# Optimization experiments

Measured on AMD Instinct MI355X. Metric: run time of the kernel, lower is better.

Reference implementation:

```python
import jax, jax.numpy as jnp
import numpy as np

B, C, H, W = 8, 32, 256, 448


def setup_inputs() -> dict:
    key = jax.random.key(0)
    k1, k2 = jax.random.split(key)
    input1 = jax.random.normal(k1, (B, C, H, W), dtype=jnp.float32)
    input2 = jax.random.normal(k2, (B, 2, H, W), dtype=jnp.float32)  # flow (u, v)
    return {"input1": input1, "input2": input2, "kernel_size": 1}


def _forward_splat(input1, input2):
    """Forward warp: splat each source pixel to (x+u, y+v) with bilinear weights,
    accumulating via scatter-add (kernel_size=1 -> 2x2 bilinear footprint)."""
    b, c, h, w = input1.shape
    u = input2[:, 0]  # [B,H,W] horizontal flow
    v = input2[:, 1]  # [B,H,W] vertical flow
    xs = jnp.arange(w, dtype=input2.dtype)
    ys = jnp.arange(h, dtype=input2.dtype)
    tx = xs[None, None, :] + u  # target x, [B,H,W]
    ty = ys[None, :, None] + v  # target y, [B,H,W]
    x0 = jnp.floor(tx).astype(jnp.int32)
    y0 = jnp.floor(ty).astype(jnp.int32)
    fx = tx - x0.astype(tx.dtype)
    fy = ty - y0.astype(ty.dtype)

    vals = input1.transpose(0, 2, 3, 1).reshape(b * h * w, c)  # [BHW, C]
    out = jnp.zeros((b * h * w, c), dtype=input1.dtype)
    batch_off = (jnp.arange(b, dtype=jnp.int32) * (h * w))[:, None, None]

    for dx, dy in ((0, 0), (1, 0), (0, 1), (1, 1)):
        xx = x0 + dx
        yy = y0 + dy
        wx = fx if dx == 1 else (1.0 - fx)
        wy = fy if dy == 1 else (1.0 - fy)
        wgt = wx * wy  # [B,H,W]
        valid = (xx >= 0) & (xx < w) & (yy >= 0) & (yy < h)
        wgt = jnp.where(valid, wgt, 0.0)
        idx = batch_off + jnp.clip(yy, 0, h - 1) * w + jnp.clip(xx, 0, w - 1)
        out = out.at[idx.reshape(-1)].add(wgt.reshape(-1, 1) * vals)

    return out.reshape(b, h, w, c).transpose(0, 3, 1, 2)


def reference(input1, input2, kernel_size):
    # kernel_size=1 corresponds to the standard bilinear (2x2) splat footprint.
    return _forward_splat(input1, input2)
```

## Files before the change

kernel.cpp:

```cpp
#include <hip/hip_runtime.h>
#include <hip/hip_fp16.h>

constexpr int B = 8;
constexpr int C = 32;
constexpr int H = 256;
constexpr int W = 448;
constexpr int HW = H * W;

constexpr int TW  = 32;
constexpr int TH  = 16;
constexpr int RAD = 3;
constexpr int WX  = TW + 2 * RAD;
constexpr int WY  = TH + 2 * RAD;
constexpr int NSRC = WX * WY;
constexpr int NT  = 512;
constexpr int SITER = (NSRC + NT - 1) / NT;

static __device__ __forceinline__ unsigned pkrtz(float a, float b) {
    return __builtin_bit_cast(unsigned, __builtin_amdgcn_cvt_pkrtz(a, b));
}

static __device__ __forceinline__ __half2 h2(unsigned u) {
    union { unsigned u; __half2 h; } x;
    x.u = u;
    return x.h;
}

__global__ __launch_bounds__(NT)
void splat_out(const float* __restrict__ in1,
               const float* __restrict__ flow,
               float* __restrict__ out,
               unsigned* __restrict__ wcnt,
               unsigned* __restrict__ wlist,
               unsigned cap) {
    __shared__ unsigned geomR[NSRC];
    __shared__ unsigned geomW[2 * NSRC];
    __shared__ uint4    valV[4 * NSRC];

    int bid = blockIdx.x;
    int b = bid & 7;
    int t = bid >> 3;
    int ty = t / 14;
    int tx = t - ty * 14;
    int ox = tx * TW, oy = ty * TH;
    int tid = threadIdx.x;
    int qlx = tid & 31, qly = tid >> 5;
    int qx = ox + qlx, qy = oy + qly;

    int sg[SITER];
    const int fbase = b * 2 * HW;
#pragma unroll
    for (int j = 0; j < SITER; ++j) {
        int i = tid + j * NT;
        if (i < NSRC) {
            int wy = i / WX, wx = i - wy * WX;
            int sx = ox + wx - RAD, sy = oy + wy - RAD;
            int cx = min(max(sx, 0), W - 1), cy = min(max(sy, 0), H - 1);
            int g = cy * W + cx;
            sg[j] = g;
            unsigned gr = 0xFFu, wlo = 0u, whi = 0u;
            if (sx == cx && sy == cy) {
                float u = flow[fbase + g];
                float v = flow[fbase + g + HW];
                float txf = (float)sx + u;
                float tyf = (float)sy + v;
                float x0f = floorf(txf), y0f = floorf(tyf);
                int rx = (int)x0f - sx, ry = (int)y0f - sy;
                if (rx >= -RAD && rx <= RAD - 1 && ry >= -RAD && ry <= RAD - 1) {
                    float fx = txf - x0f, fy = tyf - y0f;
                    wlo = pkrtz((1.f - fx) * (1.f - fy), fx * (1.f - fy));
                    whi = pkrtz((1.f - fx) * fy,         fx * fy);
                    gr = (unsigned)(rx + RAD) | ((unsigned)(ry + RAD) << 3);
                } else if (wx >= RAD && wx < RAD + TW && wy >= RAD && wy < RAD + TH) {
                    unsigned slot = atomicAdd(wcnt, 1u);
                    if (slot < cap) wlist[slot] = ((unsigned)b << 17) | (unsigned)g;
                }
            }
            geomR[i] = gr;
            geomW[2 * i]     = wlo;
            geomW[2 * i + 1] = whi;
        }
    }
    __syncthreads();

    const float* inb = in1 + (size_t)b * C * HW;
#pragma unroll
    for (int j = 0; j < SITER; ++j) {
        int i = tid + j * NT;
        if (i < NSRC) {
            const float* p = inb + sg[j];
#pragma unroll
            for (int q = 0; q < 4; ++q) {
                const float* pq = p + (size_t)(8 * q) * HW;
                uint4 vq;
                vq.x = pkrtz(pq[0],              pq[(size_t)HW]);
                vq.y = pkrtz(pq[(size_t)2 * HW], pq[(size_t)3 * HW]);
                vq.z = pkrtz(pq[(size_t)4 * HW], pq[(size_t)5 * HW]);
                vq.w = pkrtz(pq[(size_t)6 * HW], pq[(size_t)7 * HW]);
                valV[4 * i + q] = vq;
            }
        }
    }

    unsigned long long mAll = 0ull, mDx = 0ull, mDy = 0ull;
    const int qbase = (qly + RAD) * WX + (qlx + RAD);
#pragma unroll
    for (int dy = -RAD; dy <= RAD; ++dy) {
#pragma unroll
        for (int dx = -RAD; dx <= RAD; ++dx) {
            unsigned g = geomR[qbase + dy * WX + dx];
            int tX = (int)(g & 7u) + dx;
            int tY = (int)((g >> 3) & 0x1Fu) + dy;
            bool mx = (unsigned)(tX - 2) <= 1u;
            bool my = (unsigned)(tY - 2) <= 1u;
            const int j = (dy + RAD) * 8 + (dx + RAD);
            unsigned long long bit = (mx && my) ? (1ull << j) : 0ull;
            mAll |= bit;
            if (!(tX & 1)) mDx |= bit;
            if (!(tY & 1)) mDy |= bit;
        }
    }
    __syncthreads();

    __half2 acc2[16];
#pragma unroll
    for (int k = 0; k < 16; ++k) acc2[k] = h2(0u);

    const int joff = 3 * WX + 3;
    unsigned long long m = mAll;
    while (m) {
        int j = (int)__builtin_ctzll(m);
        m &= m - 1;
        int wi = qbase + ((j >> 3) * WX + (j & 7)) - joff;
        unsigned dyy = (unsigned)(mDy >> j) & 1u;
        unsigned dxx = (unsigned)(mDx >> j) & 1u;
        unsigned wd = geomW[2 * wi + dyy];
        unsigned hw = (wd >> (16u * dxx)) & 0xFFFFu;
        __half2 w2 = h2(hw | (hw << 16));
#pragma unroll
        for (int q = 0; q < 4; ++q) {
            uint4 v = valV[4 * wi + q];
            acc2[4 * q + 0] = __hfma2(h2(v.x), w2, acc2[4 * q + 0]);
            acc2[4 * q + 1] = __hfma2(h2(v.y), w2, acc2[4 * q + 1]);
            acc2[4 * q + 2] = __hfma2(h2(v.z), w2, acc2[4 * q + 2]);
            acc2[4 * q + 3] = __hfma2(h2(v.w), w2, acc2[4 * q + 3]);
        }
    }

    float* o = out + (size_t)b * C * HW + qy * W + qx;
#pragma unroll
    for (int k = 0; k < 16; ++k) {
        int c0 = 8 * (k >> 2) + 2 * (k & 3);
        float2 f = __half22float2(acc2[k]);
        o[(size_t)c0 * HW]       = f.x;
        o[(size_t)(c0 + 1) * HW] = f.y;
    }
}

__global__ void outlier_list(const float* __restrict__ in1,
                             const float* __restrict__ flow,
                             float* __restrict__ out,
                             const unsigned* __restrict__ wcnt,
                             const unsigned* __restrict__ wlist,
                             unsigned cap) {
    unsigned n = *wcnt;
    if (n > cap) return;
    unsigned total = n * 8u;
    for (unsigned idx = blockIdx.x * blockDim.x + threadIdx.x;
         idx < total; idx += gridDim.x * blockDim.x) {
        unsigned e = wlist[idx >> 3];
        int c0 = (int)(idx & 7u) * 4;
        int bb = (int)(e >> 17);
        int p  = (int)(e & 0x1FFFFu);
        int y = p / W, x = p - y * W;

        float u = flow[(bb * 2 + 0) * HW + p];
        float v = flow[(bb * 2 + 1) * HW + p];
        float txf = (float)x + u;
        float tyf = (float)y + v;
        float fx0 = floorf(txf), fy0 = floorf(tyf);
        int x0 = (int)fx0, y0 = (int)fy0;
        float fx = txf - fx0, fy = tyf - fy0;
        float w00 = (1.0f - fx) * (1.0f - fy);
        float w10 = fx * (1.0f - fy);
        float w01 = (1.0f - fx) * fy;
        float w11 = fx * fy;
        bool vx0 = (x0 >= 0) && (x0 < W);
        bool vx1 = (x0 + 1 >= 0) && (x0 + 1 < W);
        bool vy0 = (y0 >= 0) && (y0 < H);
        bool vy1 = (y0 + 1 >= 0) && (y0 + 1 < H);
        long o00 = (long)y0 * W + x0;

        const float* src  = in1 + (size_t)bb * C * HW + (size_t)c0 * HW + p;
        float*       dstb = out + (size_t)bb * C * HW + (size_t)c0 * HW;
        for (int c = 0; c < 4; ++c) {
            float val = src[(size_t)c * HW];
            float* ob = dstb + (size_t)c * HW;
            if (vx0 && vy0) atomicAdd(ob + o00,         w00 * val);
            if (vx1 && vy0) atomicAdd(ob + o00 + 1,     w10 * val);
            if (vx0 && vy1) atomicAdd(ob + o00 + W,     w01 * val);
            if (vx1 && vy1) atomicAdd(ob + o00 + W + 1, w11 * val);
        }
    }
}

__global__ void outlier_fallback(const float* __restrict__ in1,
                                 const float* __restrict__ flow,
                                 float* __restrict__ out,
                                 const unsigned* __restrict__ wcnt,
                                 unsigned cap) {
    if (*wcnt <= cap) return;
    int npix = B * HW;
    for (int idx = blockIdx.x * blockDim.x + threadIdx.x;
         idx < npix; idx += gridDim.x * blockDim.x) {
        int b = idx / HW;
        int p = idx - b * HW;
        int y = p / W, x = p - y * W;
        float u = flow[(b * 2 + 0) * HW + p];
        float v = flow[(b * 2 + 1) * HW + p];
        float txf = (float)x + u;
        float tyf = (float)y + v;
        float fx0 = floorf(txf), fy0 = floorf(tyf);
        int x0 = (int)fx0, y0 = (int)fy0;
        int rx = x0 - x, ry = y0 - y;
        bool handled = (rx >= -RAD) && (rx <= RAD - 1) &&
                       (ry >= -RAD) && (ry <= RAD - 1);
        if (handled) continue;
        float fx = txf - fx0, fy = tyf - fy0;
        float w00 = (1.0f - fx) * (1.0f - fy);
        float w10 = fx * (1.0f - fy);
        float w01 = (1.0f - fx) * fy;
        float w11 = fx * fy;
        bool vx0 = (x0 >= 0) && (x0 < W);
        bool vx1 = (x0 + 1 >= 0) && (x0 + 1 < W);
        bool vy0 = (y0 >= 0) && (y0 < H);
        bool vy1 = (y0 + 1 >= 0) && (y0 + 1 < H);
        long o00 = (long)y0 * W + x0;
        const float* src = in1 + (size_t)b * C * HW + p;
        float* dstb = out + (size_t)b * C * HW;
        for (int c = 0; c < C; ++c) {
            float val = src[(size_t)c * HW];
            float* ob = dstb + (size_t)c * HW;
            if (vx0 && vy0) atomicAdd(ob + o00,         w00 * val);
            if (vx1 && vy0) atomicAdd(ob + o00 + 1,     w10 * val);
            if (vx0 && vy1) atomicAdd(ob + o00 + W,     w01 * val);
            if (vx1 && vy1) atomicAdd(ob + o00 + W + 1, w11 * val);
        }
    }
}

extern "C" void kernel_launch(void* const* d_in, const int* in_sizes, int n_in,
                              void* d_out, int out_size, void* d_ws, size_t ws_size,
                              hipStream_t stream) {
    const float* in1  = (const float*)d_in[0];
    const float* flow = (const float*)d_in[1];
    float* out = (float*)d_out;

    unsigned* wcnt  = (unsigned*)d_ws;
    unsigned* wlist = wcnt + 4;
    unsigned cap = 0;
    if (ws_size >= 64) {
        size_t c = ws_size / sizeof(unsigned) - 4;
        cap = (c > 0x7FFFFFFFull) ? 0x7FFFFFFFu : (unsigned)c;
    }

    hipMemsetAsync(wcnt, 0, sizeof(unsigned), stream);

    int nblocks = B * (H / TH) * (W / TW);
    splat_out<<<nblocks, NT, 0, stream>>>(in1, flow, out, wcnt, wlist, cap);

    outlier_list<<<256, 256, 0, stream>>>(in1, flow, out, wcnt, wlist, cap);
    outlier_fallback<<<256, 256, 0, stream>>>(in1, flow, out, wcnt, cap);
}
```

Measured before the change: 124.0 us.

## Halve tile height, shrink shared geometry arrays, plane-major channel layout

The output tile shrinks from 32x16 to 32x8 with 256 threads per block, which raises the block count and lowers per-block shared memory so more blocks can be resident. The geometry code is stored as bytes, the two weight words are packed into a single uint2, and the half-precision channel values move from an interleaved layout to four channel-group planes, which should reduce LDS bank conflicts on the gather reads. The cost is a larger halo overhead relative to the tile (halo rows make up a bigger share of loaded sources), plus more flow and input reloads across neighbouring tiles. The grid decode elsewhere (ty = t/14) must still match the new tile count, which is not visible here.

```diff
diff --git a/kernel.cpp b/kernel.cpp
--- a/kernel.cpp
+++ b/kernel.cpp
@@ -8,12 +8,12 @@
 constexpr int HW = H * W;
 
 constexpr int TW  = 32;
-constexpr int TH  = 16;
+constexpr int TH  = 8;
 constexpr int RAD = 3;
 constexpr int WX  = TW + 2 * RAD;
 constexpr int WY  = TH + 2 * RAD;
 constexpr int NSRC = WX * WY;
-constexpr int NT  = 512;
+constexpr int NT  = 256;
 constexpr int SITER = (NSRC + NT - 1) / NT;
 
 static __device__ __forceinline__ unsigned pkrtz(float a, float b) {
@@ -33,9 +33,9 @@
                unsigned* __restrict__ wcnt,
                unsigned* __restrict__ wlist,
                unsigned cap) {
-    __shared__ unsigned geomR[NSRC];
-    __shared__ unsigned geomW[2 * NSRC];
-    __shared__ uint4    valV[4 * NSRC];
+    __shared__ unsigned char geomR8[NSRC];
+    __shared__ uint2         geomW[NSRC];
+    __shared__ uint4         valV[4 * NSRC];
 
     int bid = blockIdx.x;
     int b = bid & 7;
@@ -58,7 +58,8 @@
             int cx = min(max(sx, 0), W - 1), cy = min(max(sy, 0), H - 1);
             int g = cy * W + cx;
             sg[j] = g;
-            unsigned gr = 0xFFu, wlo = 0u, whi = 0u;
+            unsigned gr = 0xFFu;
+            uint2 wd = make_uint2(0u, 0u);
             if (sx == cx && sy == cy) {
                 float u = flow[fbase + g];
                 float v = flow[fbase + g + HW];
@@ -68,17 +69,18 @@
                 int rx = (int)x0f - sx, ry = (int)y0f - sy;
                 if (rx >= -RAD && rx <= RAD - 1 && ry >= -RAD && ry <= RAD - 1) {
                     float fx = txf - x0f, fy = tyf - y0f;
-                    wlo = pkrtz((1.f - fx) * (1.f - fy), fx * (1.f - fy));
-                    whi = pkrtz((1.f - fx) * fy,         fx * fy);
+                    wd.x = pkrtz((1.f - fx) * (1.f - fy), fx * (1.f - fy));
+                    wd.y = pkrtz((1.f - fx) * fy,         fx * fy);
                     gr = (unsigned)(rx + RAD) | ((unsigned)(ry + RAD) << 3);
                 } else if (wx >= RAD && wx < RAD + TW && wy >= RAD && wy < RAD + TH) {
                     unsigned slot = atomicAdd(wcnt, 1u);
                     if (slot < cap) wlist[slot] = ((unsigned)b << 17) | (unsigned)g;
                 }
             }
-            geomR[i] = gr;
-            geomW[2 * i]     = wlo;
-            geomW[2 * i + 1] = whi;
+            geomR8[i] = (unsigned char)gr;
+            geomW[i]  = wd;
+        } else {
+            sg[j] = -1;
         }
     }
     __syncthreads();
@@ -97,7 +99,7 @@
                 vq.y = pkrtz(pq[(size_t)2 * HW], pq[(size_t)3 * HW]);
                 vq.z = pkrtz(pq[(size_t)4 * HW], pq[(size_t)5 * HW]);
                 vq.w = pkrtz(pq[(size_t)6 * HW], pq[(size_t)7 * HW]);
-                valV[4 * i + q] = vq;
+                valV[q * NSRC + i] = vq;
             }
         }
     }
@@ -108,7 +110,7 @@
     for (int dy = -RAD; dy <= RAD; ++dy) {
 #pragma unroll
         for (int dx = -RAD; dx <= RAD; ++dx) {
-            unsigned g = geomR[qbase + dy * WX + dx];
+            unsigned g = geomR8[qbase + dy * WX + dx];
             int tX = (int)(g & 7u) + dx;
             int tY = (int)((g >> 3) & 0x1Fu) + dy;
             bool mx = (unsigned)(tX - 2) <= 1u;
@@ -134,17 +136,30 @@
         int wi = qbase + ((j >> 3) * WX + (j & 7)) - joff;
         unsigned dyy = (unsigned)(mDy >> j) & 1u;
         unsigned dxx = (unsigned)(mDx >> j) & 1u;
-        unsigned wd = geomW[2 * wi + dyy];
+        uint2 wd2 = geomW[wi];
+        unsigned wd = dyy ? wd2.y : wd2.x;
         unsigned hw = (wd >> (16u * dxx)) & 0xFFFFu;
         __half2 w2 = h2(hw | (hw << 16));
-#pragma unroll
-        for (int q = 0; q < 4; ++q) {
-            uint4 v = valV[4 * wi + q];
-            acc2[4 * q + 0] = __hfma2(h2(v.x), w2, acc2[4 * q + 0]);
-            acc2[4 * q + 1] = __hfma2(h2(v.y), w2, acc2[4 * q + 1]);
-            acc2[4 * q + 2] = __hfma2(h2(v.z), w2, acc2[4 * q + 2]);
-            acc2[4 * q + 3] = __hfma2(h2(v.w), w2, acc2[4 * q + 3]);
-        }
+        uint4 v0 = valV[0 * NSRC + wi];
+        uint4 v1 = valV[1 * NSRC + wi];
+        uint4 v2 = valV[2 * NSRC + wi];
+        uint4 v3 = valV[3 * NSRC + wi];
+        acc2[0]  = __hfma2(h2(v0.x), w2, acc2[0]);
+        acc2[1]  = __hfma2(h2(v0.y), w2, acc2[1]);
+        acc2[2]  = __hfma2(h2(v0.z), w2, acc2[2]);
+        acc2[3]  = __hfma2(h2(v0.w), w2, acc2[3]);
+        acc2[4]  = __hfma2(h2(v1.x), w2, acc2[4]);
+        acc2[5]  = __hfma2(h2(v1.y), w2, acc2[5]);
+        acc2[6]  = __hfma2(h2(v1.z), w2, acc2[6]);
+        acc2[7]  = __hfma2(h2(v1.w), w2, acc2[7]);
+        acc2[8]  = __hfma2(h2(v2.x), w2, acc2[8]);
+        acc2[9]  = __hfma2(h2(v2.y), w2, acc2[9]);
+        acc2[10] = __hfma2(h2(v2.z), w2, acc2[10]);
+        acc2[11] = __hfma2(h2(v2.w), w2, acc2[11]);
+        acc2[12] = __hfma2(h2(v3.x), w2, acc2[12]);
+        acc2[13] = __hfma2(h2(v3.y), w2, acc2[13]);
+        acc2[14] = __hfma2(h2(v3.z), w2, acc2[14]);
+        acc2[15] = __hfma2(h2(v3.w), w2, acc2[15]);
     }
 
     float* o = out + (size_t)b * C * HW + qy * W + qx;
```

Measured after the change: 115.5 us. 6.9% less time.

## Halve tile, split channels into two passes, build gather masks via shared atomics

Applied to the files above, without the earlier changes.

Shrinks the output tile to 32x8 with 256 threads and processes the 32 channels in two 16-channel passes, reusing a smaller shared staging buffer. Per-destination gather masks are now built by source threads scattering bits with shared-memory atomicOr instead of each destination scanning a 7x7 neighbourhood. The gather loop is software-pipelined so the next neighbour's weights and values are loaded before the current FMAs. The aim is lower LDS footprint and higher occupancy, at the cost of larger halo overhead per tile, extra syncs and shared atomics.

```diff
diff --git a/kernel.cpp b/kernel.cpp
--- a/kernel.cpp
+++ b/kernel.cpp
@@ -8,12 +8,12 @@
 constexpr int HW = H * W;
 
 constexpr int TW  = 32;
-constexpr int TH  = 16;
+constexpr int TH  = 8;
 constexpr int RAD = 3;
 constexpr int WX  = TW + 2 * RAD;
 constexpr int WY  = TH + 2 * RAD;
 constexpr int NSRC = WX * WY;
-constexpr int NT  = 512;
+constexpr int NT  = 256;
 constexpr int SITER = (NSRC + NT - 1) / NT;
 
 static __device__ __forceinline__ unsigned pkrtz(float a, float b) {
@@ -33,9 +33,11 @@
                unsigned* __restrict__ wcnt,
                unsigned* __restrict__ wlist,
                unsigned cap) {
-    __shared__ unsigned geomR[NSRC];
-    __shared__ unsigned geomW[2 * NSRC];
-    __shared__ uint4    valV[4 * NSRC];
+    __shared__ unsigned long long mAllS[NT];
+    __shared__ unsigned long long mDxS[NT];
+    __shared__ unsigned long long mDyS[NT];
+    __shared__ uint2 geomW[NSRC];
+    __shared__ uint4 valV[2 * NSRC];
 
     int bid = blockIdx.x;
     int b = bid & 7;
@@ -47,6 +49,11 @@
     int qlx = tid & 31, qly = tid >> 5;
     int qx = ox + qlx, qy = oy + qly;
 
+    mAllS[tid] = 0ull;
+    mDxS[tid] = 0ull;
+    mDyS[tid] = 0ull;
+    __syncthreads();
+
     int sg[SITER];
     const int fbase = b * 2 * HW;
 #pragma unroll
@@ -58,7 +65,7 @@
             int cx = min(max(sx, 0), W - 1), cy = min(max(sy, 0), H - 1);
             int g = cy * W + cx;
             sg[j] = g;
-            unsigned gr = 0xFFu, wlo = 0u, whi = 0u;
+            uint2 wd = make_uint2(0u, 0u);
             if (sx == cx && sy == cy) {
                 float u = flow[fbase + g];
                 float v = flow[fbase + g + HW];
@@ -68,93 +75,127 @@
                 int rx = (int)x0f - sx, ry = (int)y0f - sy;
                 if (rx >= -RAD && rx <= RAD - 1 && ry >= -RAD && ry <= RAD - 1) {
                     float fx = txf - x0f, fy = tyf - y0f;
-                    wlo = pkrtz((1.f - fx) * (1.f - fy), fx * (1.f - fy));
-                    whi = pkrtz((1.f - fx) * fy,         fx * fy);
-                    gr = (unsigned)(rx + RAD) | ((unsigned)(ry + RAD) << 3);
+                    wd.x = pkrtz((1.f - fx) * (1.f - fy), fx * (1.f - fy));
+                    wd.y = pkrtz((1.f - fx) * fy,         fx * fy);
+                    int lx0 = wx + rx;
+                    int ly0 = wy + ry;
+#pragma unroll
+                    for (int corner = 0; corner < 4; ++corner) {
+                        int dxx = corner & 1, dyy = corner >> 1;
+                        int ccx = lx0 + dxx - RAD;
+                        int ccy = ly0 + dyy - RAD;
+                        if ((unsigned)ccx < (unsigned)TW &&
+                            (unsigned)ccy < (unsigned)TH) {
+                            int cell = ccy * TW + ccx;
+                            unsigned long long bit =
+                                1ull << ((3 - (ry + dyy)) * 8 + (3 - (rx + dxx)));
+                            atomicOr(&mAllS[cell], bit);
+                            if (dxx) atomicOr(&mDxS[cell], bit);
+                            if (dyy) atomicOr(&mDyS[cell], bit);
+                        }
+                    }
                 } else if (wx >= RAD && wx < RAD + TW && wy >= RAD && wy < RAD + TH) {
                     unsigned slot = atomicAdd(wcnt, 1u);
                     if (slot < cap) wlist[slot] = ((unsigned)b << 17) | (unsigned)g;
                 }
             }
-            geomR[i] = gr;
-            geomW[2 * i]     = wlo;
-            geomW[2 * i + 1] = whi;
+            geomW[i] = wd;
+        } else {
+            sg[j] = -1;
         }
     }
+
+    const float* inb = in1 + (size_t)b * C * HW;
+
+    auto stage = [&](int pass) {
+#pragma unroll
+        for (int j = 0; j < SITER; ++j) {
+            int i = tid + j * NT;
+            if (i < NSRC) {
+                const float* p = inb + sg[j] + (size_t)(16 * pass) * HW;
+                valV[2 * i] = make_uint4(
+                    pkrtz(p[0],               p[(size_t)HW]),
+                    pkrtz(p[(size_t)2 * HW],  p[(size_t)3 * HW]),
+                    pkrtz(p[(size_t)4 * HW],  p[(size_t)5 * HW]),
+                    pkrtz(p[(size_t)6 * HW],  p[(size_t)7 * HW]));
+                const float* p8 = p + (size_t)8 * HW;
+                valV[2 * i + 1] = make_uint4(
+                    pkrtz(p8[0],              p8[(size_t)HW]),
+                    pkrtz(p8[(size_t)2 * HW], p8[(size_t)3 * HW]),
+                    pkrtz(p8[(size_t)4 * HW], p8[(size_t)5 * HW]),
+                    pkrtz(p8[(size_t)6 * HW], p8[(size_t)7 * HW]));
+            }
+        }
+    };
+
+    stage(0);
     __syncthreads();
 
-    const float* inb = in1 + (size_t)b * C * HW;
-#pragma unroll
-    for (int j = 0; j < SITER; ++j) {
-        int i = tid + j * NT;
-        if (i < NSRC) {
-            const float* p = inb + sg[j];
-#pragma unroll
-            for (int q = 0; q < 4; ++q) {
-                const float* pq = p + (size_t)(8 * q) * HW;
-                uint4 vq;
-                vq.x = pkrtz(pq[0],              pq[(size_t)HW]);
-                vq.y = pkrtz(pq[(size_t)2 * HW], pq[(size_t)3 * HW]);
-                vq.z = pkrtz(pq[(size_t)4 * HW], pq[(size_t)5 * HW]);
-                vq.w = pkrtz(pq[(size_t)6 * HW], pq[(size_t)7 * HW]);
-                valV[4 * i + q] = vq;
+    const unsigned long long m0  = mAllS[tid];
+    const unsigned long long mdx = mDxS[tid];
+    const unsigned long long mdy = mDyS[tid];
+    const int qbase = (qly + RAD) * WX + (qlx + RAD);
+    float* outp = out + (size_t)b * C * HW + qy * W + qx;
+
+    auto gather = [&](float* o) {
+        __half2 acc2[8];
+#pragma unroll
+        for (int k = 0; k < 8; ++k) acc2[k] = h2(0u);
+        unsigned long long m = m0;
+        if (m) {
+            int j = (int)__builtin_ctzll(m); m &= m - 1;
+            int wi = qbase + ((j >> 3) - 3) * WX + ((j & 7) - 3);
+            uint2 wdc = geomW[wi];
+            uint4 va = valV[2 * wi];
+            uint4 vb = valV[2 * wi + 1];
+            unsigned dxx = (unsigned)(mdx >> j) & 1u;
+            unsigned dyy = (unsigned)(mdy >> j) & 1u;
+            while (m) {
+                int jn = (int)__builtin_ctzll(m); m &= m - 1;
+                int win = qbase + ((jn >> 3) - 3) * WX + ((jn & 7) - 3);
+                uint2 wdn = geomW[win];
+                uint4 van = valV[2 * win];
+                uint4 vbn = valV[2 * win + 1];
+                unsigned dxxn = (unsigned)(mdx >> jn) & 1u;
+                unsigned dyyn = (unsigned)(mdy >> jn) & 1u;
+                unsigned wd = dyy ? wdc.y : wdc.x;
+                unsigned hq = (wd >> (16u * dxx)) & 0xFFFFu;
+                __half2 w2 = h2(hq | (hq << 16));
+                acc2[0] = __hfma2(h2(va.x), w2, acc2[0]);
+                acc2[1] = __hfma2(h2(va.y), w2, acc2[1]);
+                acc2[2] = __hfma2(h2(va.z), w2, acc2[2]);
+                acc2[3] = __hfma2(h2(va.w), w2, acc2[3]);
+                acc2[4] = __hfma2(h2(vb.x), w2, acc2[4]);
+                acc2[5] = __hfma2(h2(vb.y), w2, acc2[5]);
+                acc2[6] = __hfma2(h2(vb.z), w2, acc2[6]);
+                acc2[7] = __hfma2(h2(vb.w), w2, acc2[7]);
+                wdc = wdn; va = van; vb = vbn; dxx = dxxn; dyy = dyyn;
             }
-        }
-    }
-
-    unsigned long long mAll = 0ull, mDx = 0ull, mDy = 0ull;
-    const int qbase = (qly + RAD) * WX + (qlx + RAD);
-#pragma unroll
-    for (int dy = -RAD; dy <= RAD; ++dy) {
-#pragma unroll
-        for (int dx = -RAD; dx <= RAD; ++dx) {
-            unsigned g = geomR[qbase + dy * WX + dx];
-            int tX = (int)(g & 7u) + dx;
-            int tY = (int)((g >> 3) & 0x1Fu) + dy;
-            bool mx = (unsigned)(tX - 2) <= 1u;
-            bool my = (unsigned)(tY - 2) <= 1u;
-            const int j = (dy + RAD) * 8 + (dx + RAD);
-            unsigned long long bit = (mx && my) ? (1ull << j) : 0ull;
-            mAll |= bit;
-            if (!(tX & 1)) mDx |= bit;
-            if (!(tY & 1)) mDy |= bit;
-        }
-    }
+            unsigned wd = dyy ? wdc.y : wdc.x;
+            unsigned hq = (wd >> (16u * dxx)) & 0xFFFFu;
+            __half2 w2 = h2(hq | (hq << 16));
+            acc2[0] = __hfma2(h2(va.x), w2, acc2[0]);
+            acc2[1] = __hfma2(h2(va.y), w2, acc2[1]);
+            acc2[2] = __hfma2(h2(va.z), w2, acc2[2]);
+            acc2[3] = __hfma2(h2(va.w), w2, acc2[3]);
+            acc2[4] = __hfma2(h2(vb.x), w2, acc2[4]);
+            acc2[5] = __hfma2(h2(vb.y), w2, acc2[5]);
+            acc2[6] = __hfma2(h2(vb.z), w2, acc2[6]);
+            acc2[7] = __hfma2(h2(vb.w), w2, acc2[7]);
+        }
+#pragma unroll
+        for (int k = 0; k < 8; ++k) {
+            float2 f = __half22float2(acc2[k]);
+            o[(size_t)(2 * k) * HW]     = f.x;
+            o[(size_t)(2 * k + 1) * HW] = f.y;
+        }
+    };
+
+    gather(outp);
     __syncthreads();
-
-    __half2 acc2[16];
-#pragma unroll
-    for (int k = 0; k < 16; ++k) acc2[k] = h2(0u);
-
-    const int joff = 3 * WX + 3;
-    unsigned long long m = mAll;
-    while (m) {
-        int j = (int)__builtin_ctzll(m);
-        m &= m - 1;
-        int wi = qbase + ((j >> 3) * WX + (j & 7)) - joff;
-        unsigned dyy = (unsigned)(mDy >> j) & 1u;
-        unsigned dxx = (unsigned)(mDx >> j) & 1u;
-        unsigned wd = geomW[2 * wi + dyy];
-        unsigned hw = (wd >> (16u * dxx)) & 0xFFFFu;
-        __half2 w2 = h2(hw | (hw << 16));
-#pragma unroll
-        for (int q = 0; q < 4; ++q) {
-            uint4 v = valV[4 * wi + q];
-            acc2[4 * q + 0] = __hfma2(h2(v.x), w2, acc2[4 * q + 0]);
-            acc2[4 * q + 1] = __hfma2(h2(v.y), w2, acc2[4 * q + 1]);
-            acc2[4 * q + 2] = __hfma2(h2(v.z), w2, acc2[4 * q + 2]);
-            acc2[4 * q + 3] = __hfma2(h2(v.w), w2, acc2[4 * q + 3]);
-        }
-    }
-
-    float* o = out + (size_t)b * C * HW + qy * W + qx;
-#pragma unroll
-    for (int k = 0; k < 16; ++k) {
-        int c0 = 8 * (k >> 2) + 2 * (k & 3);
-        float2 f = __half22float2(acc2[k]);
-        o[(size_t)c0 * HW]       = f.x;
-        o[(size_t)(c0 + 1) * HW] = f.y;
-    }
+    stage(1);
+    __syncthreads();
+    gather(outp + (size_t)16 * HW);
 }
 
 __global__ void outlier_list(const float* __restrict__ in1,
```

Result: faster. 112.9 us (-9.0%).
